# Kernel optimization log

Hardware: AMD Instinct MI355X
Metric: run time of the kernel (lower is better)

## Reference

```python
import itertools
import jax, jax.numpy as jnp
import numpy as np

N_OBJECTS = 32
GRAPHLET_SIZE = 3
N_FILTERS = 16
REL_DIM = 16
BATCH = 32
N_GROUP_QUERIES = 512
BETA = 1.0

# static combinatorial groups: all C(32,3) = 4960 index triples
GROUP_IDX = jnp.asarray(
    np.array(list(itertools.combinations(range(N_OBJECTS), GRAPHLET_SIZE)), dtype=np.int32)
)  # (G, g)


def setup_inputs() -> dict:
    key = jax.random.key(0)
    k1, k2, k3 = jax.random.split(key, 3)
    inputs = jax.random.normal(k1, (BATCH, N_OBJECTS, N_OBJECTS, REL_DIM), dtype=jnp.float32)
    group_logits = jax.random.normal(k2, (N_GROUP_QUERIES, N_OBJECTS), dtype=jnp.float32)
    filters = jax.random.normal(k3, (N_FILTERS, GRAPHLET_SIZE, GRAPHLET_SIZE, REL_DIM), dtype=jnp.float32)
    return {"inputs": inputs, "group_logits": group_logits, "filters": filters}


def reference(inputs, group_logits, filters):
    idx = GROUP_IDX  # (G, g)
    # gather sub-relation tensors for every group in one fused advanced-index:
    # (B, G, g, g, D)
    sub_rel = inputs[:, idx[:, :, None], idx[:, None, :], :]
    # relational inner product with all filters: (B, G, F)
    rel_conv = jnp.einsum('bgijd,fijd->bgf', sub_rel, filters)
    # soft group weights
    sp = jax.nn.softplus(group_logits)            # (Gi, N)
    group_obj_w = sp[:, idx]                      # (Gi, G, g) -- gather along object axis
    group_w = jnp.prod(group_obj_w, axis=-1)      # (Gi, G)
    norm_w = jax.nn.softmax(BETA * group_w, axis=-1)  # (Gi, G)
    # contract over combinatorial groups: (B, Gi, F)
    out = jnp.einsum('bnr,gn->bgr', rel_conv, norm_w)
    return out
```

## Files before the change

kernel.cpp:

```cpp
#include <hip/hip_runtime.h>
#include <hip/hip_bf16.h>

#define N_OBJ   32
#define G_TOTAL 4960
#define GPAD    5120
#define N_FILT  16
#define REL_D   16
#define BATCH   32
#define NQ      512
#define ZSPLIT  16
#define KCH     320
#define NIT     10

typedef __attribute__((ext_vector_type(8))) short bf16x8;
typedef __attribute__((ext_vector_type(4))) float f32x4;

static __device__ inline unsigned short f2bf(float x) {
    union { float f; unsigned int u; } v; v.f = x;
    unsigned int r = v.u + 0x7fffu + ((v.u >> 16) & 1u);
    return (unsigned short)(r >> 16);
}
static __device__ inline float bfbits2f(unsigned int bits) {
    union { unsigned int u; float f; } v; v.u = bits; return v.f;
}
static __device__ inline void gload_lds16(const void* g, void* l) {
    __builtin_amdgcn_global_load_lds(
        (const __attribute__((address_space(1))) unsigned int*)g,
        (__attribute__((address_space(3))) unsigned int*)(unsigned int)(uintptr_t)l,
        16, 0, 0);
}
static __device__ inline void unrank3(int g, int& a, int& b, int& c) {
    int rem = g;
    for (a = 0; a < 30; a++) { int cnt = ((31 - a) * (30 - a)) >> 1; if (rem < cnt) break; rem -= cnt; }
    for (b = a + 1; b < 31; b++) { if (rem < 31 - b) break; rem -= 31 - b; }
    c = b + 1 + rem;
}

__global__ __launch_bounds__(256) void k_front(const float* __restrict__ logits,
                                               const float* __restrict__ inputs,
                                               const float* __restrict__ filters,
                                               unsigned short* __restrict__ normw,
                                               unsigned short* __restrict__ D) {
    __shared__ __align__(16) char smem[11648];
    int t = threadIdx.x;
    int role = blockIdx.x;

    if (role < NQ) {
        float* sp  = (float*)smem;
        float* red = (float*)(smem + 128);
        unsigned short* wrow = (unsigned short*)(smem + 144);
        int q = role;
        if (t < N_OBJ) {
            float x = logits[q * N_OBJ + t];
            sp[t] = (x > 15.f) ? x : log1pf(expf(x));
        }
        if (t < GPAD - G_TOTAL) wrow[G_TOTAL + t] = 0;
        __syncthreads();

        int g0 = t * 20;
        int aa, bb, cc;
        unrank3(g0, aa, bb, cc);

        float w[20];
        float lmax = -1e30f;
#pragma unroll
        for (int k = 0; k < 20; k++) {
            float v = -1e30f;
            if (g0 + k < G_TOTAL) v = sp[aa] * sp[bb] * sp[cc];
            w[k] = v;
            lmax = fmaxf(lmax, v);
            cc++;
            if (cc >= 32) { bb++; cc = bb + 1; if (cc >= 32) { aa++; bb = aa + 1; cc = bb + 1; } }
        }
#pragma unroll
        for (int off = 32; off; off >>= 1) lmax = fmaxf(lmax, __shfl_down(lmax, off, 64));
        if ((t & 63) == 0) red[t >> 6] = lmax;
        __syncthreads();
        float wmax = fmaxf(fmaxf(red[0], red[1]), fmaxf(red[2], red[3]));

        float lsum = 0.f;
#pragma unroll
        for (int k = 0; k < 20; k++) {
            float e = (g0 + k < G_TOTAL) ? expf(w[k] - wmax) : 0.f;
            w[k] = e;
            lsum += e;
        }
#pragma unroll
        for (int off = 32; off; off >>= 1) lsum += __shfl_down(lsum, off, 64);
        __syncthreads();
        if ((t & 63) == 0) red[t >> 6] = lsum;
        __syncthreads();
        float inv = 1.f / (red[0] + red[1] + red[2] + red[3]);

#pragma unroll
        for (int k = 0; k < 20; k++)
            if (g0 + k < G_TOTAL) wrow[g0 + k] = f2bf(w[k] * inv);
        __syncthreads();
        uint4* dstrow = (uint4*)(normw + (size_t)q * GPAD);
        const uint4* srow = (const uint4*)wrow;
        for (int i = t; i < 640; i += 256) dstrow[i] = srow[i];
    } else {
        float* flt = (float*)smem;
        int bid = role - NQ;
        int p = bid >> 7;
        int xb = bid & 127;
        for (int i = t; i < 576; i += 256) {
            int i4 = i * 4;
            int f = i4 / 144;
            int r = i4 - f * 144;
            *(float4*)&flt[f * 180 + (r >> 4) * 20 + (r & 15)] = *(const float4*)(filters + i4);
        }
        __syncthreads();

        int row = xb * 256 + t;
        int b = row >> 10, xy = row & 1023;
        const float4* src = (const float4*)(inputs + (size_t)row * 16);
        float4 s0 = src[0], s1 = src[1], s2 = src[2], s3 = src[3];

        unsigned short outv[16];
        const float* fb = &flt[p * 20];
#pragma unroll
        for (int f = 0; f < 16; f++) {
            float4 f0 = *(const float4*)(fb + f * 180);
            float4 f1 = *(const float4*)(fb + f * 180 + 4);
            float4 f2 = *(const float4*)(fb + f * 180 + 8);
            float4 f3 = *(const float4*)(fb + f * 180 + 12);
            float d = s0.x * f0.x + s0.y * f0.y + s0.z * f0.z + s0.w * f0.w;
            d += s1.x * f1.x + s1.y * f1.y + s1.z * f1.z + s1.w * f1.w;
            d += s2.x * f2.x + s2.y * f2.y + s2.z * f2.z + s2.w * f2.w;
            d += s3.x * f3.x + s3.y * f3.y + s3.z * f3.z + s3.w * f3.w;
            outv[f] = f2bf(d);
        }
        uint4* dst = (uint4*)(D + ((size_t)(xy * 9 + p)) * 512 + b * 16);
        dst[0] = ((uint4*)outv)[0];
        dst[1] = ((uint4*)outv)[1];
    }
}

__global__ __launch_bounds__(256) void k_mid(const unsigned short* __restrict__ D,
                                             unsigned short* __restrict__ relT) {
    __shared__ int tri[8];
    int t = threadIdx.x;
    int g0 = blockIdx.x * 8;
    if (t < 8) {
        int a, b, c;
        unrank3(g0 + t, a, b, c);
        tri[t] = a | (b << 8) | (c << 16);
    }
    __syncthreads();

    float s0[8], s1[8];
#pragma unroll
    for (int g = 0; g < 8; g++) {
        int pk = tri[g];
        int xs[3] = { pk & 255, (pk >> 8) & 255, (pk >> 16) & 255 };
        float x0 = 0.f, x1 = 0.f;
#pragma unroll
        for (int i = 0; i < 3; i++)
#pragma unroll
            for (int j = 0; j < 3; j++) {
                int xy = xs[i] * 32 + xs[j];
                unsigned int v = *(const unsigned int*)(D + (size_t)(xy * 9 + i * 3 + j) * 512 + t * 2);
                x0 += bfbits2f(v << 16);
                x1 += bfbits2f(v & 0xffff0000u);
            }
        s0[g] = x0; s1[g] = x1;
    }
    unsigned int pack0[4], pack1[4];
#pragma unroll
    for (int k = 0; k < 4; k++) {
        pack0[k] = f2bf(s0[2 * k]) | ((unsigned int)f2bf(s0[2 * k + 1]) << 16);
        pack1[k] = f2bf(s1[2 * k]) | ((unsigned int)f2bf(s1[2 * k + 1]) << 16);
    }
    *(uint4*)(relT + (size_t)(2 * t) * GPAD + g0)     = *(uint4*)pack0;
    *(uint4*)(relT + (size_t)(2 * t + 1) * GPAD + g0) = *(uint4*)pack1;
}

__global__ __launch_bounds__(256) void k_gemm(const unsigned short* __restrict__ A,
                                              const unsigned short* __restrict__ Bm,
                                              float* __restrict__ part) {
    __shared__ __align__(16) unsigned short As[2][64 * 32];
    __shared__ __align__(16) unsigned short Bs[2][64 * 32];
    int tid = threadIdx.x;
    int q0 = blockIdx.x * 64, n0 = blockIdx.y * 64, z = blockIdx.z;
    int k0 = z * KCH;
    int wave = tid >> 6, lane = tid & 63;
    int wm = wave & 1, wn = wave >> 1;
    int row16 = lane & 15, quad = lane >> 4;

    int srow = tid >> 2;
    int schunk = (tid & 3) ^ ((srow >> 1) & 3);
    const unsigned short* ga = A + (size_t)(q0 + srow) * GPAD + k0 + schunk * 8;
    const unsigned short* gb = Bm + (size_t)(n0 + srow) * GPAD + k0 + schunk * 8;
    char* lA = (char*)&As[0][0] + tid * 16;
    char* lB = (char*)&Bs[0][0] + tid * 16;

    f32x4 acc[2][2] = {};
    int fchunk = (quad ^ ((row16 >> 1) & 3)) * 8;

    gload_lds16(ga, lA);
    gload_lds16(gb, lB);
    for (int it = 0; it < NIT; ++it) {
        __syncthreads();
        if (it + 1 < NIT) {
            int nb = (it + 1) & 1;
            gload_lds16(ga + (it + 1) * 32, lA + nb * 64 * 32 * 2);
            gload_lds16(gb + (it + 1) * 32, lB + nb * 64 * 32 * 2);
        }
        int buf = it & 1;
        bf16x8 afr[2], bfr[2];
#pragma unroll
        for (int mi = 0; mi < 2; mi++)
            afr[mi] = *(const bf16x8*)&As[buf][(wm * 32 + mi * 16 + row16) * 32 + fchunk];
#pragma unroll
        for (int ni = 0; ni < 2; ni++)
            bfr[ni] = *(const bf16x8*)&Bs[buf][(wn * 32 + ni * 16 + row16) * 32 + fchunk];
#pragma unroll
        for (int mi = 0; mi < 2; mi++)
#pragma unroll
            for (int ni = 0; ni < 2; ni++)
                acc[mi][ni] = __builtin_amdgcn_mfma_f32_16x16x32_bf16(
                    afr[mi], bfr[ni], acc[mi][ni], 0, 0, 0);
    }

    float* pz = part + (size_t)z * (NQ * 512);
#pragma unroll
    for (int mi = 0; mi < 2; mi++)
#pragma unroll
        for (int ni = 0; ni < 2; ni++)
#pragma unroll
            for (int r = 0; r < 4; r++) {
                int q = q0 + wm * 32 + mi * 16 + quad * 4 + r;
                int n = n0 + wn * 32 + ni * 16 + row16;
                pz[q * 512 + n] = acc[mi][ni][r];
            }
}

__global__ __launch_bounds__(256) void k_reduce(const float* __restrict__ part,
                                                float* __restrict__ out) {
    int gid = blockIdx.x * 256 + threadIdx.x;
    int q = gid >> 7;
    int n = (gid & 127) * 4;
    float4 a = *(const float4*)(part + q * 512 + n);
#pragma unroll
    for (int zz = 1; zz < ZSPLIT; zz++) {
        float4 b4 = *(const float4*)(part + (size_t)zz * (NQ * 512) + q * 512 + n);
        a.x += b4.x; a.y += b4.y; a.z += b4.z; a.w += b4.w;
    }
    *(float4*)(out + (size_t)(n >> 4) * (NQ * REL_D) + q * 16 + (n & 15)) = a;
}

extern "C" void kernel_launch(void* const* d_in, const int* in_sizes, int n_in,
                              void* d_out, int out_size, void* d_ws, size_t ws_size,
                              hipStream_t stream) {
    const float* inputs  = (const float*)d_in[0];
    const float* logits  = (const float*)d_in[1];
    const float* filters = (const float*)d_in[2];
    float* out = (float*)d_out;

    char* ws = (char*)d_ws;
    unsigned short* normw = (unsigned short*)ws;
    unsigned short* D     = (unsigned short*)(ws + 5242880);
    unsigned short* relT  = (unsigned short*)(ws + 14680064);
    float*          part  = (float*)(ws + 19922944);

    k_front<<<NQ + 1152, 256, 0, stream>>>(logits, inputs, filters, normw, D);
    k_mid<<<G_TOTAL / 8, 256, 0, stream>>>(D, relT);
    k_gemm<<<dim3(8, 8, ZSPLIT), 256, 0, stream>>>(normw, relT, part);
    k_reduce<<<NQ * 512 / 4 / 256, 256, 0, stream>>>(part, out);
}
```

Baseline: 94.91 us.

## Fuse split-K reduction into GEMM via last-arriver atomic counter; halve split-K

Drops the separate reduce kernel. Each GEMM tile block increments a per-tile counter after storing its partial, and the last block to arrive sums all split-K partials and writes the output. The counters are zeroed by an extra block added to the mid kernel. Split-K is cut from 16 to 8, which halves partial traffic but leaves fewer blocks (512 instead of 1024) for the GEMM, and the final reduction runs serially inside one block per tile.

```diff
diff --git a/kernel.cpp b/kernel.cpp
--- a/kernel.cpp
+++ b/kernel.cpp
@@ -8,9 +8,9 @@
 #define REL_D   16
 #define BATCH   32
 #define NQ      512
-#define ZSPLIT  16
-#define KCH     320
-#define NIT     10
+#define ZSPLIT  8
+#define KCH     640
+#define NIT     20
 
 typedef __attribute__((ext_vector_type(8))) short bf16x8;
 typedef __attribute__((ext_vector_type(4))) float f32x4;
@@ -138,10 +138,16 @@
 }
 
 __global__ __launch_bounds__(256) void k_mid(const unsigned short* __restrict__ D,
-                                             unsigned short* __restrict__ relT) {
+                                             unsigned short* __restrict__ relT,
+                                             int* __restrict__ cnt) {
     __shared__ int tri[8];
     int t = threadIdx.x;
-    int g0 = blockIdx.x * 8;
+    int role = blockIdx.x;
+    if (role >= 620) {
+        if (t < 64) cnt[t] = 0;
+        return;
+    }
+    int g0 = role * 8;
     if (t < 8) {
         int a, b, c;
         unrank3(g0 + t, a, b, c);
@@ -176,11 +182,14 @@
     *(uint4*)(relT + (size_t)(2 * t + 1) * GPAD + g0) = *(uint4*)pack1;
 }
 
-__global__ __launch_bounds__(256) void k_gemm(const unsigned short* __restrict__ A,
-                                              const unsigned short* __restrict__ Bm,
-                                              float* __restrict__ part) {
+__global__ __launch_bounds__(256) void k_gemmred(const unsigned short* __restrict__ A,
+                                                 const unsigned short* __restrict__ Bm,
+                                                 float* __restrict__ part,
+                                                 int* __restrict__ cnt,
+                                                 float* __restrict__ out) {
     __shared__ __align__(16) unsigned short As[2][64 * 32];
     __shared__ __align__(16) unsigned short Bs[2][64 * 32];
+    __shared__ int isfix;
     int tid = threadIdx.x;
     int q0 = blockIdx.x * 64, n0 = blockIdx.y * 64, z = blockIdx.z;
     int k0 = z * KCH;
@@ -234,20 +243,29 @@
                 int n = n0 + wn * 32 + ni * 16 + row16;
                 pz[q * 512 + n] = acc[mi][ni][r];
             }
-}
-
-__global__ __launch_bounds__(256) void k_reduce(const float* __restrict__ part,
-                                                float* __restrict__ out) {
-    int gid = blockIdx.x * 256 + threadIdx.x;
-    int q = gid >> 7;
-    int n = (gid & 127) * 4;
-    float4 a = *(const float4*)(part + q * 512 + n);
-#pragma unroll
-    for (int zz = 1; zz < ZSPLIT; zz++) {
-        float4 b4 = *(const float4*)(part + (size_t)zz * (NQ * 512) + q * 512 + n);
-        a.x += b4.x; a.y += b4.y; a.z += b4.z; a.w += b4.w;
-    }
-    *(float4*)(out + (size_t)(n >> 4) * (NQ * REL_D) + q * 16 + (n & 15)) = a;
+
+    __threadfence();
+    __syncthreads();
+    if (tid == 0) {
+        int old = atomicAdd(&cnt[blockIdx.x * 8 + blockIdx.y], 1);
+        isfix = (old == ZSPLIT - 1);
+    }
+    __syncthreads();
+    if (!isfix) return;
+
+    int n = tid & 63;
+    int qrow = tid >> 6;
+#pragma unroll
+    for (int pass = 0; pass < 16; pass++) {
+        int q = q0 + pass * 4 + qrow;
+        float s = 0.f;
+#pragma unroll
+        for (int zz = 0; zz < ZSPLIT; zz++)
+            s += __hip_atomic_load(part + (size_t)zz * (NQ * 512) + q * 512 + n0 + n,
+                                   __ATOMIC_RELAXED, __HIP_MEMORY_SCOPE_AGENT);
+        int nn = n0 + n;
+        out[(size_t)(nn >> 4) * (NQ * REL_D) + q * 16 + (nn & 15)] = s;
+    }
 }
 
 extern "C" void kernel_launch(void* const* d_in, const int* in_sizes, int n_in,
@@ -263,9 +281,9 @@
     unsigned short* D     = (unsigned short*)(ws + 5242880);
     unsigned short* relT  = (unsigned short*)(ws + 14680064);
     float*          part  = (float*)(ws + 19922944);
+    int*            cnt   = (int*)(ws + 28311552);
 
     k_front<<<NQ + 1152, 256, 0, stream>>>(logits, inputs, filters, normw, D);
-    k_mid<<<G_TOTAL / 8, 256, 0, stream>>>(D, relT);
-    k_gemm<<<dim3(8, 8, ZSPLIT), 256, 0, stream>>>(normw, relT, part);
-    k_reduce<<<NQ * 512 / 4 / 256, 256, 0, stream>>>(part, out);
-}
+    k_mid<<<621, 256, 0, stream>>>(D, relT, cnt);
+    k_gemmred<<<dim3(8, 8, ZSPLIT), 256, 0, stream>>>(normw, relT, part, cnt, out);
+}
```

Measured after the change: 154.1 us. +62.4%, slower.

## Fuse split-K reduction into GEMM via intra-block wave K-split

Applied to the files above, without the earlier changes.

Replaces the global split-K GEMM (16 z-slices writing fp32 partials) and the separate reduce kernel with a single kernel. Each block computes a 32x32 output tile, and each of its four waves handles a quarter of K using its own double-buffered LDS region and per-wave waitcnt instead of block barriers. Partials are summed through LDS and written directly to the output. This removes the partial-buffer global traffic and one kernel launch. In exchange the grid shrinks to 256 blocks, and each wave runs a longer serial K loop of 40 iterations.

```diff
diff --git a/kernel.cpp b/kernel.cpp
--- a/kernel.cpp
+++ b/kernel.cpp
@@ -8,9 +8,8 @@
 #define REL_D   16
 #define BATCH   32
 #define NQ      512
-#define ZSPLIT  16
-#define KCH     320
-#define NIT     10
+#define KWAVE   1280
+#define NIT     40
 
 typedef __attribute__((ext_vector_type(8))) short bf16x8;
 typedef __attribute__((ext_vector_type(4))) float f32x4;
@@ -176,78 +175,76 @@
     *(uint4*)(relT + (size_t)(2 * t + 1) * GPAD + g0) = *(uint4*)pack1;
 }
 
-__global__ __launch_bounds__(256) void k_gemm(const unsigned short* __restrict__ A,
-                                              const unsigned short* __restrict__ Bm,
-                                              float* __restrict__ part) {
-    __shared__ __align__(16) unsigned short As[2][64 * 32];
-    __shared__ __align__(16) unsigned short Bs[2][64 * 32];
+__global__ __launch_bounds__(256) void k_gemmf(const unsigned short* __restrict__ A,
+                                               const unsigned short* __restrict__ Bm,
+                                               float* __restrict__ out) {
+    __shared__ __align__(16) char smem[32768];
     int tid = threadIdx.x;
-    int q0 = blockIdx.x * 64, n0 = blockIdx.y * 64, z = blockIdx.z;
-    int k0 = z * KCH;
     int wave = tid >> 6, lane = tid & 63;
-    int wm = wave & 1, wn = wave >> 1;
+    int q0 = blockIdx.x * 32, n0 = blockIdx.y * 32;
     int row16 = lane & 15, quad = lane >> 4;
 
-    int srow = tid >> 2;
-    int schunk = (tid & 3) ^ ((srow >> 1) & 3);
-    const unsigned short* ga = A + (size_t)(q0 + srow) * GPAD + k0 + schunk * 8;
-    const unsigned short* gb = Bm + (size_t)(n0 + srow) * GPAD + k0 + schunk * 8;
-    char* lA = (char*)&As[0][0] + tid * 16;
-    char* lB = (char*)&Bs[0][0] + tid * 16;
+    int srow = lane >> 2;
+    int schunk = (lane & 3) ^ ((srow >> 1) & 3);
+    const unsigned short* gA = A  + (size_t)(q0 + srow) * GPAD + wave * KWAVE + schunk * 8;
+    const unsigned short* gB = Bm + (size_t)(n0 + srow) * GPAD + wave * KWAVE + schunk * 8;
+    char* lw = smem + wave * 8192;
+    char* ld = lw + lane * 16;
 
     f32x4 acc[2][2] = {};
-    int fchunk = (quad ^ ((row16 >> 1) & 3)) * 8;
-
-    gload_lds16(ga, lA);
-    gload_lds16(gb, lB);
+    int fslot = (quad ^ ((row16 >> 1) & 3)) * 16;
+
+    gload_lds16(gA,             ld);
+    gload_lds16(gA + 16 * GPAD, ld + 1024);
+    gload_lds16(gB,             ld + 2048);
+    gload_lds16(gB + 16 * GPAD, ld + 3072);
+
+#pragma unroll 2
     for (int it = 0; it < NIT; ++it) {
-        __syncthreads();
+        int buf = it & 1;
+        asm volatile("s_waitcnt vmcnt(0)" ::: "memory");
+        const char* fb = lw + buf * 4096;
+        bf16x8 a0 = *(const bf16x8*)(fb + row16 * 64 + fslot);
+        bf16x8 a1 = *(const bf16x8*)(fb + 1024 + row16 * 64 + fslot);
+        bf16x8 b0 = *(const bf16x8*)(fb + 2048 + row16 * 64 + fslot);
+        bf16x8 b1 = *(const bf16x8*)(fb + 3072 + row16 * 64 + fslot);
+        asm volatile("s_waitcnt lgkmcnt(0)" ::: "memory");
         if (it + 1 < NIT) {
-            int nb = (it + 1) & 1;
-            gload_lds16(ga + (it + 1) * 32, lA + nb * 64 * 32 * 2);
-            gload_lds16(gb + (it + 1) * 32, lB + nb * 64 * 32 * 2);
-        }
-        int buf = it & 1;
-        bf16x8 afr[2], bfr[2];
-#pragma unroll
-        for (int mi = 0; mi < 2; mi++)
-            afr[mi] = *(const bf16x8*)&As[buf][(wm * 32 + mi * 16 + row16) * 32 + fchunk];
+            int ko = (it + 1) * 32;
+            char* ln = ld + (buf ^ 1) * 4096;
+            gload_lds16(gA + ko,             ln);
+            gload_lds16(gA + 16 * GPAD + ko, ln + 1024);
+            gload_lds16(gB + ko,             ln + 2048);
+            gload_lds16(gB + 16 * GPAD + ko, ln + 3072);
+        }
+        acc[0][0] = __builtin_amdgcn_mfma_f32_16x16x32_bf16(a0, b0, acc[0][0], 0, 0, 0);
+        acc[0][1] = __builtin_amdgcn_mfma_f32_16x16x32_bf16(a0, b1, acc[0][1], 0, 0, 0);
+        acc[1][0] = __builtin_amdgcn_mfma_f32_16x16x32_bf16(a1, b0, acc[1][0], 0, 0, 0);
+        acc[1][1] = __builtin_amdgcn_mfma_f32_16x16x32_bf16(a1, b1, acc[1][1], 0, 0, 0);
+    }
+
+    __syncthreads();
+    float* red = (float*)smem;
+#pragma unroll
+    for (int mi = 0; mi < 2; mi++)
 #pragma unroll
         for (int ni = 0; ni < 2; ni++)
-            bfr[ni] = *(const bf16x8*)&Bs[buf][(wn * 32 + ni * 16 + row16) * 32 + fchunk];
-#pragma unroll
-        for (int mi = 0; mi < 2; mi++)
-#pragma unroll
-            for (int ni = 0; ni < 2; ni++)
-                acc[mi][ni] = __builtin_amdgcn_mfma_f32_16x16x32_bf16(
-                    afr[mi], bfr[ni], acc[mi][ni], 0, 0, 0);
-    }
-
-    float* pz = part + (size_t)z * (NQ * 512);
-#pragma unroll
-    for (int mi = 0; mi < 2; mi++)
-#pragma unroll
-        for (int ni = 0; ni < 2; ni++)
-#pragma unroll
-            for (int r = 0; r < 4; r++) {
-                int q = q0 + wm * 32 + mi * 16 + quad * 4 + r;
-                int n = n0 + wn * 32 + ni * 16 + row16;
-                pz[q * 512 + n] = acc[mi][ni][r];
-            }
-}
-
-__global__ __launch_bounds__(256) void k_reduce(const float* __restrict__ part,
-                                                float* __restrict__ out) {
-    int gid = blockIdx.x * 256 + threadIdx.x;
-    int q = gid >> 7;
-    int n = (gid & 127) * 4;
-    float4 a = *(const float4*)(part + q * 512 + n);
-#pragma unroll
-    for (int zz = 1; zz < ZSPLIT; zz++) {
-        float4 b4 = *(const float4*)(part + (size_t)zz * (NQ * 512) + q * 512 + n);
-        a.x += b4.x; a.y += b4.y; a.z += b4.z; a.w += b4.w;
-    }
-    *(float4*)(out + (size_t)(n >> 4) * (NQ * REL_D) + q * 16 + (n & 15)) = a;
+#pragma unroll
+            for (int r = 0; r < 4; r++)
+                red[wave * 1024 + (mi * 16 + quad * 4 + r) * 32 + ni * 16 + row16] =
+                    acc[mi][ni][r];
+    __syncthreads();
+
+    int e = tid * 4;
+    float4 s = *(const float4*)&red[e];
+#pragma unroll
+    for (int w = 1; w < 4; w++) {
+        float4 v = *(const float4*)&red[w * 1024 + e];
+        s.x += v.x; s.y += v.y; s.z += v.z; s.w += v.w;
+    }
+    int ql = e >> 5, nl = e & 31;
+    int nn = n0 + nl;
+    *(float4*)(out + (size_t)(nn >> 4) * (NQ * REL_D) + (q0 + ql) * 16 + (nn & 15)) = s;
 }
 
 extern "C" void kernel_launch(void* const* d_in, const int* in_sizes, int n_in,
@@ -262,10 +259,8 @@
     unsigned short* normw = (unsigned short*)ws;
     unsigned short* D     = (unsigned short*)(ws + 5242880);
     unsigned short* relT  = (unsigned short*)(ws + 14680064);
-    float*          part  = (float*)(ws + 19922944);
 
     k_front<<<NQ + 1152, 256, 0, stream>>>(logits, inputs, filters, normw, D);
     k_mid<<<G_TOTAL / 8, 256, 0, stream>>>(D, relT);
-    k_gemm<<<dim3(8, 8, ZSPLIT), 256, 0, stream>>>(normw, relT, part);
-    k_reduce<<<NQ * 512 / 4 / 256, 256, 0, stream>>>(part, out);
-}
+    k_gemmf<<<dim3(16, 16), 256, 0, stream>>>(normw, relT, out);
+}
```

Result: slower. 97.62 us (+2.9%).
